# Performance work log

Measured on AMD Instinct MI355X. Metric: run time of the kernel, lower is better.

The kernel has to match this reference:

```python
import jax, jax.numpy as jnp
import numpy as np
import math

N_HEAD = 16
ROPE_BASE = 10000.0


def _rope_cos_sin(seq_len, head_dim, dtype):
    # standard RoPE tables: freqs_i = base^(-2i/d), i in [0, d/2)
    half = head_dim // 2
    inv_freq = ROPE_BASE ** (-(jnp.arange(half, dtype=jnp.float32) * 2.0 / head_dim))
    t = jnp.arange(seq_len, dtype=jnp.float32)
    ang = t[:, None] * inv_freq[None, :]  # [S, d/2]
    return jnp.cos(ang).astype(dtype), jnp.sin(ang).astype(dtype)


def _apply_rope(x, cos, sin):
    # x: [B, S, H, d]; rotate interleaved even/odd pairs
    x1 = x[..., 0::2]
    x2 = x[..., 1::2]
    c = cos[None, :, None, :]
    s = sin[None, :, None, :]
    out = jnp.stack([x1 * c - x2 * s, x1 * s + x2 * c], axis=-1)
    return out.reshape(x.shape)


def setup_inputs() -> dict:
    key = jax.random.key(0)
    kx, kq, kk, kv, ko = jax.random.split(key, 5)
    B, S, H = 2, 2048, 1024
    x = jax.random.normal(kx, (B, S, H), dtype=jnp.float32)
    scale = 0.02
    w_q = jax.random.normal(kq, (H, H), dtype=jnp.float32) * scale
    w_k = jax.random.normal(kk, (H, H), dtype=jnp.float32) * scale
    w_v = jax.random.normal(kv, (H, H), dtype=jnp.float32) * scale
    w_o = jax.random.normal(ko, (H, H), dtype=jnp.float32) * scale
    return {"x": x, "w_q": w_q, "w_k": w_k, "w_v": w_v, "w_o": w_o}


def reference(x, w_q, w_k, w_v, w_o):
    B, S, H = x.shape
    d = H // N_HEAD
    # torch nn.Linear(bias=False): y = x @ W^T, W is [out, in]
    q = (x @ w_q.T).reshape(B, S, N_HEAD, d)
    k = (x @ w_k.T).reshape(B, S, N_HEAD, d)
    v = (x @ w_v.T).reshape(B, S, N_HEAD, d)
    cos, sin = _rope_cos_sin(S, d, x.dtype)
    q = _apply_rope(q, cos, sin)
    k = _apply_rope(k, cos, sin)
    scores = jnp.einsum("bqhd,bkhd->bhqk", q, k) / math.sqrt(d)
    coefs = jax.nn.softmax(scores, axis=-1)
    # NOTE: causal mask is applied AFTER softmax via tril (no renormalization)
    causal = jnp.tril(jnp.ones((S, S), dtype=bool))
    coefs = jnp.where(causal[None, None], coefs, 0.0)
    out = jnp.einsum("bhqk,bkhd->bqhd", coefs, v).reshape(B, S, H)
    return out @ w_o.T
```

## Files before the change

kernel.cpp:

```cpp
#include <hip/hip_runtime.h>
#include <math.h>

#define SEQ   2048
#define HDIM  1024
#define NH    16
#define DH    64
#define MTOT  4096
#define BHTOT 32

typedef _Float16 half_t;
typedef __attribute__((ext_vector_type(2))) __fp16 fp16x2;
typedef __attribute__((ext_vector_type(4))) _Float16 half4;
typedef __attribute__((ext_vector_type(8))) _Float16 half8;
typedef __attribute__((ext_vector_type(4))) float float4v;

typedef __attribute__((address_space(1))) const unsigned int guint;
typedef __attribute__((address_space(3))) unsigned int luint;
__device__ __forceinline__ void glds16(const half_t* g, half_t* l) {
    __builtin_amdgcn_global_load_lds((guint*)g, (luint*)l, 16, 0, 0);
}

__global__ __launch_bounds__(256)
void prep(const float* __restrict__ x,  const float* __restrict__ wq,
          const float* __restrict__ wk, const float* __restrict__ wv,
          const float* __restrict__ wo,
          half_t* __restrict__ xh,  half_t* __restrict__ wqh,
          half_t* __restrict__ wkh, half_t* __restrict__ wvh,
          half_t* __restrict__ woh, float2* __restrict__ rope)
{
    const int bid = blockIdx.x;
    if (bid < 8192) {
        int i = bid * 256 + threadIdx.x;
        const float* s; half_t* d;
        if (i < 1048576) { s = x; d = xh; }
        else {
            int j = i - 1048576;
            int w = j >> 18; i = j & 262143;
            s = (w == 0) ? wq : (w == 1) ? wk : (w == 2) ? wv : wo;
            d = (w == 0) ? wqh : (w == 1) ? wkh : (w == 2) ? wvh : woh;
        }
        float4 v = ((const float4*)s)[i];
        union { half_t h[4]; uint2 u; } tmp;
        tmp.h[0] = (half_t)v.x; tmp.h[1] = (half_t)v.y;
        tmp.h[2] = (half_t)v.z; tmp.h[3] = (half_t)v.w;
        ((uint2*)d)[i] = tmp.u;
    } else {
        int tt = (bid - 8192) * 256 + threadIdx.x;
        int s = tt >> 5, j = tt & 31;
        float inv = powf(10000.0f, -(float)j / 32.0f);
        float ang = (float)s * inv;
        rope[tt] = make_float2(cosf(ang), sinf(ang));
    }
}

__global__ __launch_bounds__(256, 5)
void gemm_qkv(const half_t* __restrict__ A,
              const half_t* __restrict__ w0, const half_t* __restrict__ w1,
              const half_t* __restrict__ w2,
              half_t* __restrict__ Qb, half_t* __restrict__ Kb,
              half_t* __restrict__ Vtb,
              const float2* __restrict__ rope)
{
    const int mode = blockIdx.z;
    const half_t* Bw = (mode == 1) ? w1 : (mode == 2) ? w2 : w0;

    __shared__ __align__(16) half_t Tsh[2][128][64];
    half_t (*Ash)[64] = Tsh[0];
    half_t (*Bsh)[64] = Tsh[1];

    const int t    = threadIdx.x;
    const int lane = t & 63;
    const int wave = t >> 6;
    const int quad = lane >> 4;
    const int l16  = lane & 15;
    const int wr   = (wave >> 1) * 64;
    const int wc   = (wave & 1) * 64;
    const int bm   = blockIdx.x, bn = blockIdx.y;

    const int srow   = lane >> 3;
    const int schunk = (lane & 7) ^ (srow & 3);
    const half_t* Asrc = A  + (size_t)(bm * 128 + srow) * HDIM + schunk * 8;
    const half_t* Bsrc = Bw + (size_t)(bn * 128 + srow) * HDIM + schunk * 8;
    const int swz = (l16 & 3) << 4;

    float4v acc[4][4] = {};

    for (int kt = 0; kt < HDIM / 64; ++kt) {
        const half_t* Ak = Asrc + kt * 64;
        const half_t* Bk = Bsrc + kt * 64;
#pragma unroll
        for (int c = 0; c < 4; ++c) {
            const int r8 = wave * 32 + c * 8;
            glds16(Ak + (size_t)r8 * HDIM, &Ash[r8][0]);
            glds16(Bk + (size_t)r8 * HDIM, &Bsh[r8][0]);
        }
        __syncthreads();
#pragma unroll
        for (int kk = 0; kk < 2; ++kk) {
            const int cb = ((quad << 4) | (kk << 6)) ^ swz;
            half8 af[4], bf[4];
#pragma unroll
            for (int mb = 0; mb < 4; ++mb)
                af[mb] = *(const half8*)((const char*)&Ash[wr + mb * 16 + l16][0] + cb);
#pragma unroll
            for (int nb = 0; nb < 4; ++nb)
                bf[nb] = *(const half8*)((const char*)&Bsh[wc + nb * 16 + l16][0] + cb);
#pragma unroll
            for (int mb = 0; mb < 4; ++mb)
#pragma unroll
                for (int nb = 0; nb < 4; ++nb)
                    acc[mb][nb] = __builtin_amdgcn_mfma_f32_16x16x32_f16(af[mb], bf[nb], acc[mb][nb], 0, 0, 0);
        }
        __syncthreads();
    }

    if (mode == 2) {
#pragma unroll
        for (int mb = 0; mb < 4; ++mb)
#pragma unroll
            for (int nb = 0; nb < 4; ++nb) {
                int row0 = bm * 128 + wr + mb * 16 + quad * 4;
                int col  = bn * 128 + wc + nb * 16 + l16;
                int b = row0 >> 11, s0 = row0 & 2047;
                int h = col >> 6,  dd = col & 63;
                union { half_t h4[4]; uint2 u; } tmp;
#pragma unroll
                for (int r = 0; r < 4; ++r) tmp.h4[r] = (half_t)acc[mb][nb][r];
                *(uint2*)&Vtb[((size_t)((b * NH + h) * DH + dd)) * SEQ + s0] = tmp.u;
            }
        return;
    }
    {
        half_t* Ob = (mode == 0) ? Qb : Kb;
        const float scl = (mode == 0) ? 0.125f * 1.44269504088896f : 1.0f;
        const int h = (bn * 128 + wc) >> 6;
        float* E = (float*)&Tsh[0][0][0] + wave * 1088;
#pragma unroll
        for (int mb = 0; mb < 4; ++mb) {
#pragma unroll
            for (int nb = 0; nb < 4; ++nb)
#pragma unroll
                for (int r = 0; r < 4; ++r)
                    E[(quad * 4 + r) * 68 + nb * 16 + l16] = acc[mb][nb][r];
            __asm__ volatile("s_waitcnt lgkmcnt(0)" ::: "memory");
#pragma unroll
            for (int c = 0; c < 2; ++c) {
                const int uidx = c * 64 + lane;
                const int row = uidx >> 3, ch = uidx & 7;
                const int sg = bm * 128 + wr + mb * 16 + row;
                const int b = sg >> 11, s = sg & 2047;
                const float* Er = E + row * 68 + ch * 8;
                const float4 e0 = *(const float4*)Er;
                const float4 e1 = *(const float4*)(Er + 4);
                const float4* rp = (const float4*)(rope + (size_t)s * 32 + ch * 4);
                const float4 r01 = rp[0];
                const float4 r23 = rp[1];
                union { half_t hh[8]; uint4 u; } o;
                o.hh[0] = (half_t)((e0.x * r01.x - e0.y * r01.y) * scl);
                o.hh[1] = (half_t)((e0.x * r01.y + e0.y * r01.x) * scl);
                o.hh[2] = (half_t)((e0.z * r01.z - e0.w * r01.w) * scl);
                o.hh[3] = (half_t)((e0.z * r01.w + e0.w * r01.z) * scl);
                o.hh[4] = (half_t)((e1.x * r23.x - e1.y * r23.y) * scl);
                o.hh[5] = (half_t)((e1.x * r23.y + e1.y * r23.x) * scl);
                o.hh[6] = (half_t)((e1.z * r23.z - e1.w * r23.w) * scl);
                o.hh[7] = (half_t)((e1.z * r23.w + e1.w * r23.z) * scl);
                *(uint4*)&Ob[((size_t)((b * NH + h) * SEQ + s)) * DH + ch * 8] = o.u;
            }
        }
    }
}

__global__ __launch_bounds__(256)
void gemm_out(const half_t* __restrict__ A, const half_t* __restrict__ W,
              float* __restrict__ outF)
{
    __shared__ __align__(16) half_t Ash[64][64];
    __shared__ __align__(16) half_t Bsh[128][64];

    const int t    = threadIdx.x;
    const int lane = t & 63;
    const int wave = t >> 6;
    const int quad = lane >> 4;
    const int l16  = lane & 15;
    const int wr   = (wave >> 1) * 32;
    const int wc   = (wave & 1) * 64;
    const int bm   = blockIdx.x, bn = blockIdx.y;

    const int srow   = lane >> 3;
    const int schunk = (lane & 7) ^ (srow & 3);
    const half_t* Asrc = A + (size_t)(bm * 64  + srow) * HDIM + schunk * 8;
    const half_t* Bsrc = W + (size_t)(bn * 128 + srow) * HDIM + schunk * 8;
    const int swz = (l16 & 3) << 4;

    float4v acc[2][4] = {};

    for (int kt = 0; kt < HDIM / 64; ++kt) {
        const half_t* Ak = Asrc + kt * 64;
        const half_t* Bk = Bsrc + kt * 64;
#pragma unroll
        for (int c = 0; c < 2; ++c) {
            const int r8 = wave * 16 + c * 8;
            glds16(Ak + (size_t)r8 * HDIM, &Ash[r8][0]);
        }
#pragma unroll
        for (int c = 0; c < 4; ++c) {
            const int r8 = wave * 32 + c * 8;
            glds16(Bk + (size_t)r8 * HDIM, &Bsh[r8][0]);
        }
        __syncthreads();
#pragma unroll
        for (int kk = 0; kk < 2; ++kk) {
            const int cb = ((quad << 4) | (kk << 6)) ^ swz;
            half8 af[2], bf[4];
#pragma unroll
            for (int mb = 0; mb < 2; ++mb)
                af[mb] = *(const half8*)((const char*)&Ash[wr + mb * 16 + l16][0] + cb);
#pragma unroll
            for (int nb = 0; nb < 4; ++nb)
                bf[nb] = *(const half8*)((const char*)&Bsh[wc + nb * 16 + l16][0] + cb);
#pragma unroll
            for (int mb = 0; mb < 2; ++mb)
#pragma unroll
                for (int nb = 0; nb < 4; ++nb)
                    acc[mb][nb] = __builtin_amdgcn_mfma_f32_16x16x32_f16(af[mb], bf[nb], acc[mb][nb], 0, 0, 0);
        }
        __syncthreads();
    }

#pragma unroll
    for (int mb = 0; mb < 2; ++mb)
#pragma unroll
        for (int nb = 0; nb < 4; ++nb) {
            int row0 = bm * 64 + wr + mb * 16 + quad * 4;
            int col  = bn * 128 + wc + nb * 16 + l16;
#pragma unroll
            for (int r = 0; r < 4; ++r)
                outF[(size_t)(row0 + r) * HDIM + col] = acc[mb][nb][r];
        }
}

__global__ __launch_bounds__(512, 4)
void attn_fused(const half_t* __restrict__ Qb, const half_t* __restrict__ Kb,
                const half_t* __restrict__ Vtb, half_t* __restrict__ AOut)
{
    const int bx = blockIdx.x;
    const int p  = bx >> 1;
    const int hf = bx & 1;
    const int bh = blockIdx.y;

    __shared__ __align__(16) half_t Ksh[2][64][64];
    __shared__ __align__(16) half_t Vsh[2][64][72];

    const int t = threadIdx.x;
    const int wave = t >> 6, lane = t & 63, quad = lane >> 4, l16 = lane & 15;
    const int heavy = wave >> 2, wl = wave & 3;
    const int qtile = heavy ? (15 - p) : p;
    const int q0 = qtile * 128 + hf * 64 + wl * 16;
    const int ktop = 2 * (15 - p) + hf;

    const half_t* Qp = Qb + ((size_t)bh * SEQ + q0 + l16) * DH + quad * 8;
    const half8 qf0 = *(const half8*)Qp;
    const half8 qf1 = *(const half8*)(Qp + 32);

    float4v o[4] = {};
    float4v ls = {};

    const int krow = lane >> 3, kpos = lane & 7;
    const int kchunk = kpos ^ krow;
    const half_t* Ksrc = Kb + ((size_t)bh * SEQ + wave * 8 + krow) * DH + kchunk * 8;
    const int ko1 = ((quad ^ (l16 & 7)) * 8);
    const int ko2 = ko1 ^ 32;

    const int sr  = t >> 3;
    const int scc = (t & 7) * 8;
    const half_t* Vg = Vtb + ((size_t)bh * DH + sr) * SEQ + scc;

    glds16(Ksrc, &Ksh[0][wave * 8][0]);
    *(uint4*)&Vsh[0][sr][scc] = *(const uint4*)(Vg);
    __syncthreads();

    for (int kt = 0; kt < SEQ / 64; ++kt) {
        const int cur = kt & 1, nxt = cur ^ 1;
        const bool have_next = (kt + 1 < SEQ / 64);
        const bool next_v    = (kt + 1 <= ktop);

        if (have_next)
            glds16(Ksrc + (size_t)(kt + 1) * 64 * DH, &Ksh[nxt][wave * 8][0]);
        uint4 va;
        if (have_next && next_v)
            va = *(const uint4*)(Vg + (kt + 1) * 64);

        float4v sc[4];
        __builtin_amdgcn_s_setprio(1);
#pragma unroll
        for (int nb = 0; nb < 4; ++nb) {
            const half_t* kp = &Ksh[cur][nb * 16 + l16][0];
            half8 kf0 = *(const half8*)(kp + ko1);
            half8 kf1 = *(const half8*)(kp + ko2);
            float4v a = {};
            a = __builtin_amdgcn_mfma_f32_16x16x32_f16(kf0, qf0, a, 0, 0, 0);
            a = __builtin_amdgcn_mfma_f32_16x16x32_f16(kf1, qf1, a, 0, 0, 0);
            sc[nb] = a;
        }
        __builtin_amdgcn_s_setprio(0);

#pragma unroll
        for (int nb = 0; nb < 4; ++nb)
#pragma unroll
            for (int r = 0; r < 4; ++r) {
                float e = __builtin_amdgcn_exp2f(sc[nb][r]);
                sc[nb][r] = e;
                ls[r] += e;
            }

        const int kbase = kt * 64;
        if (kbase <= q0 + 15) {
            if (kbase + 63 > q0) {
                int qg = q0 + l16;
#pragma unroll
                for (int nb = 0; nb < 4; ++nb)
#pragma unroll
                    for (int r = 0; r < 4; ++r)
                        if (kbase + nb * 16 + quad * 4 + r > qg) sc[nb][r] = 0.f;
            }
            half4 pf[4];
#pragma unroll
            for (int nb = 0; nb < 4; ++nb) {
                union { fp16x2 v2[2]; half4 v4; } u;
                u.v2[0] = __builtin_amdgcn_cvt_pkrtz(sc[nb][0], sc[nb][1]);
                u.v2[1] = __builtin_amdgcn_cvt_pkrtz(sc[nb][2], sc[nb][3]);
                pf[nb] = u.v4;
            }
            __builtin_amdgcn_s_setprio(1);
#pragma unroll
            for (int md = 0; md < 4; ++md)
#pragma unroll
                for (int nb = 0; nb < 4; ++nb) {
                    half4 vf = *(const half4*)&Vsh[cur][md * 16 + l16][nb * 16 + quad * 4];
                    o[md] = __builtin_amdgcn_mfma_f32_16x16x16f16(vf, pf[nb], o[md], 0, 0, 0);
                }
            __builtin_amdgcn_s_setprio(0);
        }

        if (have_next && next_v)
            *(uint4*)&Vsh[nxt][sr][scc] = va;
        __syncthreads();
    }

    const int b = bh >> 4, h = bh & 15;
    const int orow = lane >> 2, occ = (lane & 3) * 16;
    half_t* scr = (heavy ? (half_t*)Vsh : (half_t*)Ksh) + wl * 1152;
    half_t (*Osh)[72] = (half_t(*)[72])scr;
    {
        float rs = (ls[0] + ls[1]) + (ls[2] + ls[3]);
        rs += __shfl_xor(rs, 16, 64);
        rs += __shfl_xor(rs, 32, 64);
        const float inv = 1.0f / rs;
#pragma unroll
        for (int md = 0; md < 4; ++md)
#pragma unroll
            for (int r = 0; r < 4; ++r)
                Osh[l16][md * 16 + quad * 4 + r] = (half_t)(o[md][r] * inv);
        __asm__ volatile("s_waitcnt lgkmcnt(0)" ::: "memory");
        uint4 o0 = *(const uint4*)&Osh[orow][occ];
        uint4 o1 = *(const uint4*)&Osh[orow][occ + 8];
        const int s = q0 + orow;
        half_t* dst = AOut + ((size_t)(b * SEQ + s)) * HDIM + h * DH + occ;
        *(uint4*)dst       = o0;
        *(uint4*)(dst + 8) = o1;
    }
}

extern "C" void kernel_launch(void* const* d_in, const int* in_sizes, int n_in,
                              void* d_out, int out_size, void* d_ws, size_t ws_size,
                              hipStream_t stream)
{
    const float* x  = (const float*)d_in[0];
    const float* wq = (const float*)d_in[1];
    const float* wk = (const float*)d_in[2];
    const float* wv = (const float*)d_in[3];
    const float* wo = (const float*)d_in[4];
    float* out = (float*)d_out;

    char* ws = (char*)d_ws;
    size_t off = 0;
    auto alloc = [&](size_t bytes) -> void* {
        void* p = ws + off;
        off += (bytes + 255) & ~(size_t)255;
        return p;
    };
    half_t* xh   = (half_t*)alloc((size_t)MTOT * HDIM * 2);
    half_t* wqh  = (half_t*)alloc((size_t)HDIM * HDIM * 2);
    half_t* wkh  = (half_t*)alloc((size_t)HDIM * HDIM * 2);
    half_t* wvh  = (half_t*)alloc((size_t)HDIM * HDIM * 2);
    half_t* woh  = (half_t*)alloc((size_t)HDIM * HDIM * 2);
    half_t* Qb   = (half_t*)alloc((size_t)BHTOT * SEQ * DH * 2);
    half_t* Kb   = (half_t*)alloc((size_t)BHTOT * SEQ * DH * 2);
    half_t* Vtb  = (half_t*)alloc((size_t)BHTOT * SEQ * DH * 2);
    half_t* ah   = (half_t*)alloc((size_t)MTOT * HDIM * 2);
    float2* rope = (float2*)alloc((size_t)SEQ * 32 * sizeof(float2));

    prep<<<8448, 256, 0, stream>>>(x, wq, wk, wv, wo, xh, wqh, wkh, wvh, woh, rope);

    gemm_qkv<<<dim3(32, 8, 3), 256, 0, stream>>>(xh, wqh, wkh, wvh,
                                                 Qb, Kb, Vtb, rope);
    attn_fused<<<dim3(16, 32), 512, 0, stream>>>(Qb, Kb, Vtb, ah);
    gemm_out<<<dim3(64, 8), 256, 0, stream>>>(ah, woh, out);
}
```

Before: 187.3 us.

## Double-buffer out-projection GEMM and triple-buffer K with swizzled V in attention

The output-projection GEMM now double-buffers its A/B LDS tiles, so the next k-tile loads while the current one is multiplied. The attention kernel gains a third K buffer to prefetch two tiles ahead. It also stores V in an XOR-swizzled 64-wide layout instead of padding to 72. Full __syncthreads are replaced by explicit vmcnt/lgkmcnt waits plus s_barrier. This hides global-load latency and cuts LDS bank conflicts, at the cost of more LDS per block and fragile hand-written wait counts that may limit occupancy.

Result: no change. 188.7 us (+0.7%).

```diff
diff --git a/kernel.cpp b/kernel.cpp
--- a/kernel.cpp
+++ b/kernel.cpp
@@ -174,8 +174,8 @@
 void gemm_out(const half_t* __restrict__ A, const half_t* __restrict__ W,
               float* __restrict__ outF)
 {
-    __shared__ __align__(16) half_t Ash[64][64];
-    __shared__ __align__(16) half_t Bsh[128][64];
+    __shared__ __align__(16) half_t Ash[2][64][64];
+    __shared__ __align__(16) half_t Bsh[2][128][64];
 
     const int t    = threadIdx.x;
     const int lane = t & 63;
@@ -192,39 +192,50 @@
     const half_t* Bsrc = W + (size_t)(bn * 128 + srow) * HDIM + schunk * 8;
     const int swz = (l16 & 3) << 4;
 
-    float4v acc[2][4] = {};
-
-    for (int kt = 0; kt < HDIM / 64; ++kt) {
+    auto stage = [&](int kt, int buf) {
         const half_t* Ak = Asrc + kt * 64;
         const half_t* Bk = Bsrc + kt * 64;
 #pragma unroll
         for (int c = 0; c < 2; ++c) {
             const int r8 = wave * 16 + c * 8;
-            glds16(Ak + (size_t)r8 * HDIM, &Ash[r8][0]);
+            glds16(Ak + (size_t)r8 * HDIM, &Ash[buf][r8][0]);
         }
 #pragma unroll
         for (int c = 0; c < 4; ++c) {
             const int r8 = wave * 32 + c * 8;
-            glds16(Bk + (size_t)r8 * HDIM, &Bsh[r8][0]);
-        }
-        __syncthreads();
+            glds16(Bk + (size_t)r8 * HDIM, &Bsh[buf][r8][0]);
+        }
+    };
+
+    float4v acc[2][4] = {};
+
+    stage(0, 0);
+    __asm__ volatile("s_waitcnt vmcnt(0)" ::: "memory");
+    __builtin_amdgcn_s_barrier();
+    __builtin_amdgcn_sched_barrier(0);
+
+    for (int kt = 0; kt < HDIM / 64; ++kt) {
+        const int cur = kt & 1, nxt = cur ^ 1;
+        if (kt + 1 < HDIM / 64) stage(kt + 1, nxt);
 #pragma unroll
         for (int kk = 0; kk < 2; ++kk) {
             const int cb = ((quad << 4) | (kk << 6)) ^ swz;
             half8 af[2], bf[4];
 #pragma unroll
             for (int mb = 0; mb < 2; ++mb)
-                af[mb] = *(const half8*)((const char*)&Ash[wr + mb * 16 + l16][0] + cb);
+                af[mb] = *(const half8*)((const char*)&Ash[cur][wr + mb * 16 + l16][0] + cb);
 #pragma unroll
             for (int nb = 0; nb < 4; ++nb)
-                bf[nb] = *(const half8*)((const char*)&Bsh[wc + nb * 16 + l16][0] + cb);
+                bf[nb] = *(const half8*)((const char*)&Bsh[cur][wc + nb * 16 + l16][0] + cb);
 #pragma unroll
             for (int mb = 0; mb < 2; ++mb)
 #pragma unroll
                 for (int nb = 0; nb < 4; ++nb)
                     acc[mb][nb] = __builtin_amdgcn_mfma_f32_16x16x32_f16(af[mb], bf[nb], acc[mb][nb], 0, 0, 0);
         }
-        __syncthreads();
+        __asm__ volatile("s_waitcnt vmcnt(0)" ::: "memory");
+        __builtin_amdgcn_s_barrier();
+        __builtin_amdgcn_sched_barrier(0);
     }
 
 #pragma unroll
@@ -247,9 +258,10 @@
     const int p  = bx >> 1;
     const int hf = bx & 1;
     const int bh = blockIdx.y;
-
-    __shared__ __align__(16) half_t Ksh[2][64][64];
-    __shared__ __align__(16) half_t Vsh[2][64][72];
+    const int NT = SEQ / 64;
+
+    __shared__ __align__(16) half_t Ksh[3][64][64];
+    __shared__ __align__(16) half_t Vsh[2][64][64];
 
     const int t = threadIdx.x;
     const int wave = t >> 6, lane = t & 63, quad = lane >> 4, l16 = lane & 15;
@@ -272,29 +284,35 @@
     const int ko2 = ko1 ^ 32;
 
     const int sr  = t >> 3;
-    const int scc = (t & 7) * 8;
-    const half_t* Vg = Vtb + ((size_t)bh * DH + sr) * SEQ + scc;
-
-    glds16(Ksrc, &Ksh[0][wave * 8][0]);
-    *(uint4*)&Vsh[0][sr][scc] = *(const uint4*)(Vg);
-    __syncthreads();
-
-    for (int kt = 0; kt < SEQ / 64; ++kt) {
-        const int cur = kt & 1, nxt = cur ^ 1;
-        const bool have_next = (kt + 1 < SEQ / 64);
-        const bool next_v    = (kt + 1 <= ktop);
-
-        if (have_next)
-            glds16(Ksrc + (size_t)(kt + 1) * 64 * DH, &Ksh[nxt][wave * 8][0]);
-        uint4 va;
-        if (have_next && next_v)
-            va = *(const uint4*)(Vg + (kt + 1) * 64);
+    const int svc = ((t & 7) ^ (sr & 7)) * 8;
+    const half_t* Vg = Vtb + ((size_t)bh * DH + sr) * SEQ + (t & 7) * 8;
+    const int vxo = l16 & 7;
+    const int vro = (quad & 1) * 8;
+
+    uint4 va = *(const uint4*)(Vg);
+    glds16(Ksrc,                   &Ksh[0][wave * 8][0]);
+    glds16(Ksrc + (size_t)64 * DH, &Ksh[1][wave * 8][0]);
+    *(uint4*)&Vsh[0][sr][svc] = va;
+    __asm__ volatile("s_waitcnt vmcnt(1)" ::: "memory");
+    __asm__ volatile("s_waitcnt lgkmcnt(0)" ::: "memory");
+    __builtin_amdgcn_s_barrier();
+    __builtin_amdgcn_sched_barrier(0);
+
+    int i0 = 0, i1 = 1, i2 = 2;
+    for (int kt = 0; kt < NT; ++kt) {
+        const int curv = kt & 1, nxtv = curv ^ 1;
+        const bool vnext = (kt + 1 <= ktop) && (kt + 1 < NT);
+        const bool knext = (kt + 2 < NT);
+
+        if (vnext) va = *(const uint4*)(Vg + (kt + 1) * 64);
+        if (knext)
+            glds16(Ksrc + (size_t)(kt + 2) * 64 * DH, &Ksh[i2][wave * 8][0]);
 
         float4v sc[4];
         __builtin_amdgcn_s_setprio(1);
 #pragma unroll
         for (int nb = 0; nb < 4; ++nb) {
-            const half_t* kp = &Ksh[cur][nb * 16 + l16][0];
+            const half_t* kp = &Ksh[i0][nb * 16 + l16][0];
             half8 kf0 = *(const half8*)(kp + ko1);
             half8 kf1 = *(const half8*)(kp + ko2);
             float4v a = {};
@@ -333,18 +351,25 @@
             }
             __builtin_amdgcn_s_setprio(1);
 #pragma unroll
-            for (int md = 0; md < 4; ++md)
+            for (int md = 0; md < 4; ++md) {
+                const char* vrow = (const char*)&Vsh[curv][md * 16 + l16][0];
 #pragma unroll
                 for (int nb = 0; nb < 4; ++nb) {
-                    half4 vf = *(const half4*)&Vsh[cur][md * 16 + l16][nb * 16 + quad * 4];
+                    const int sco = (((nb * 2 + (quad >> 1)) ^ vxo) << 4) + vro;
+                    half4 vf = *(const half4*)(vrow + sco);
                     o[md] = __builtin_amdgcn_mfma_f32_16x16x16f16(vf, pf[nb], o[md], 0, 0, 0);
                 }
+            }
             __builtin_amdgcn_s_setprio(0);
         }
 
-        if (have_next && next_v)
-            *(uint4*)&Vsh[nxt][sr][scc] = va;
-        __syncthreads();
+        if (vnext) *(uint4*)&Vsh[nxtv][sr][svc] = va;
+        if (knext) { __asm__ volatile("s_waitcnt vmcnt(1)" ::: "memory"); }
+        else       { __asm__ volatile("s_waitcnt vmcnt(0)" ::: "memory"); }
+        __asm__ volatile("s_waitcnt lgkmcnt(0)" ::: "memory");
+        __builtin_amdgcn_s_barrier();
+        __builtin_amdgcn_sched_barrier(0);
+        const int tmp = i0; i0 = i1; i1 = i2; i2 = tmp;
     }
 
     const int b = bh >> 4, h = bh & 15;
```
